# Optimization experiments

Measured on AMD Instinct MI355X. Metric: run time of the kernel, lower is better.

The kernel has to match this reference:

```python
import jax, jax.numpy as jnp
import numpy as np

NEG_SLOPE = 0.2  # PyG GATv2Conv default negative_slope


def setup_inputs() -> dict:
    key = jax.random.key(0)
    ks = jax.random.split(key, 8)
    B, N, C, H, F, E = 16, 5000, 128, 2, 64, 1_280_000
    T = B * N
    s = 0.05
    x = jax.random.normal(ks[0], (B, N, C), jnp.float32)
    edge_index = jax.random.randint(ks[1], (2, E), 0, T, jnp.int32)
    Wl = jax.random.normal(ks[2], (C, H * F), jnp.float32) * s
    bl = jnp.zeros((H * F,), jnp.float32)
    Wr = jax.random.normal(ks[3], (C, H * F), jnp.float32) * s
    br = jnp.zeros((H * F,), jnp.float32)
    att = jax.random.normal(ks[4], (H, F), jnp.float32) * s
    bias = jnp.zeros((H * F,), jnp.float32)
    return {"x": x, "edge_index": edge_index, "Wl": Wl, "bl": bl,
            "Wr": Wr, "br": br, "att": att, "bias": bias}


def reference(x, edge_index, Wl, bl, Wr, br, att, bias):
    # x: (B, N, C) -> flatten to (T, C), T = B*N total nodes
    B, N, C = x.shape
    T = B * N
    H, F = att.shape
    xf = x.reshape(T, C)
    x_l = (xf @ Wl + bl).reshape(T, H, F)  # source transform (lin_l)
    x_r = (xf @ Wr + br).reshape(T, H, F)  # target transform (lin_r)
    # add self loops (add_self_loops=True)
    loops = jnp.arange(T, dtype=edge_index.dtype)
    src = jnp.concatenate([edge_index[0], loops])
    dst = jnp.concatenate([edge_index[1], loops])
    # GATv2 score: att . LeakyReLU(x_j + x_i)
    e = jax.nn.leaky_relu(x_l[src] + x_r[dst], NEG_SLOPE)  # (Et, H, F)
    logits = jnp.einsum('ehf,hf->eh', e, att)              # (Et, H)
    # edge softmax over incoming edges of each dst node
    m = jax.lax.stop_gradient(jax.ops.segment_max(logits, dst, num_segments=T))
    p = jnp.exp(logits - m[dst])
    denom = jax.ops.segment_sum(p, dst, num_segments=T)
    alpha = p / denom[dst]                                  # (Et, H)
    # aggregate: out_i = sum_j alpha_ij * x_l[j]
    out = jax.ops.segment_sum(x_l[src] * alpha[:, :, None], dst, num_segments=T)
    out = out.reshape(T, H * F) + bias  # concat=True -> (T, H*F)
    return out.reshape(B, N, H * F)
```

## Files before the change

kernel.cpp:

```cpp
#include <hip/hip_runtime.h>
#include <hip/hip_bf16.h>

typedef __hip_bfloat16 bf16;
typedef short s16x8 __attribute__((ext_vector_type(8)));
typedef float f32x4 __attribute__((ext_vector_type(4)));
typedef float f32x2 __attribute__((ext_vector_type(2)));

#define NEG_SLOPE 0.2f
#define MAXB 160
#define EPB  4096
#define SCAP 10240
#define TRS  132

__device__ __forceinline__ unsigned int f32_to_bf16_bits(float f) {
    unsigned int u = __float_as_uint(f);
    return (u + 0x7FFFu + ((u >> 16) & 1u)) >> 16;
}
__device__ __forceinline__ float bf16lo_to_f32(unsigned int u) {
    return __uint_as_float(u << 16);
}
__device__ __forceinline__ float bf16hi_to_f32(unsigned int u) {
    return __uint_as_float(u & 0xFFFF0000u);
}
__device__ __forceinline__ float loadf_rt(const void* p, size_t i, int isb) {
    return isb ? __bfloat162float(((const bf16*)p)[i]) : ((const float*)p)[i];
}

#define ROR_ADD(v, n)                                                          \
    v += __int_as_float(__builtin_amdgcn_update_dpp(                           \
        0, __float_as_int(v), 0x120 + (n), 0xF, 0xF, true))

__global__ void prep_w(const unsigned short* __restrict__ xh,
                       const void* __restrict__ Wl, const void* __restrict__ Wr,
                       unsigned short* __restrict__ bpack,
                       int* __restrict__ flag, int* __restrict__ g2)
{
    if (blockIdx.x == 16) {
        int tid = threadIdx.x;
        for (int j = tid; j < 2 * MAXB; j += 256) g2[j] = 0;
        unsigned short h = xh[tid & 255];
        int e = (h >> 7) & 0xFF;
        int c = ((h & 0x7FFF) == 0 || (e >= 117 && e <= 131)) ? 1 : 0;
        __shared__ int sc[4];
        int lane = tid & 63, wid = tid >> 6;
        #pragma unroll
        for (int off = 32; off; off >>= 1) c += __shfl_xor(c, off, 64);
        if (lane == 0) sc[wid] = c;
        __syncthreads();
        if (tid == 0) *flag = ((sc[0] + sc[1] + sc[2] + sc[3]) >= 4 * 192) ? 1 : 0;
        return;
    }

    __shared__ int s_isb;
    {
        int tl = threadIdx.x;
        if (tl < 64) {
            int cnt = 0;
            for (int j = tl; j < 256; j += 64) {
                unsigned short h = xh[j];
                int e = (h >> 7) & 0xFF;
                if ((h & 0x7FFF) == 0 || (e >= 117 && e <= 131)) cnt++;
            }
            #pragma unroll
            for (int off = 32; off; off >>= 1) cnt += __shfl_xor(cnt, off, 64);
            if (tl == 0) s_isb = (cnt >= 192) ? 1 : 0;
        }
        __syncthreads();
    }
    int isb = s_isb;

    int tid = blockIdx.x * 256 + threadIdx.x;
    int lane = tid & 63;
    int kc   = (tid >> 6) & 3;
    int nt   = (tid >> 8) & 7;
    int mat  = tid >> 11;
    const void* W = mat ? Wr : Wl;
    int n  = nt * 16 + (lane & 15);
    int k0 = kc * 32 + (lane >> 4) * 8;
    unsigned short* o = bpack + (size_t)tid * 8;
    #pragma unroll
    for (int j = 0; j < 8; ++j)
        o[j] = (unsigned short)f32_to_bf16_bits(loadf_rt(W, (size_t)(k0 + j) * 128 + n, isb));
}

__global__ void gemm_or_scatter(const void* __restrict__ x,
                                const unsigned short* __restrict__ bpack,
                                const void* __restrict__ bl, const void* __restrict__ br,
                                unsigned int* __restrict__ xlp, unsigned int* __restrict__ xrp,
                                int T, const int* __restrict__ flag,
                                const int* __restrict__ ei, int E, int Et,
                                int nbuck, int Gg, int* __restrict__ delta,
                                unsigned int* __restrict__ packed)
{
    __shared__ unsigned int smem[4][16][TRS];

    if ((int)blockIdx.x >= Gg) {
        int* h   = (int*)&smem[0][0][0];
        int* cur = h + 4 * MAXB;
        int sb  = blockIdx.x - Gg;
        int tid = threadIdx.x, wid = tid >> 6;
        for (int j = tid; j < 4 * MAXB; j += 256) h[j] = 0;
        __syncthreads();
        int start = sb * EPB;
        int end   = min(start + EPB, Et);
        for (int i = start + tid; i < end; i += 256) {
            int dst = (i < E) ? ei[E + i] : (i - E);
            atomicAdd(&h[wid * MAXB + (dst >> 9)], 1);
        }
        __syncthreads();
        for (int b = tid; b < nbuck; b += 256) {
            int c = h[0 * MAXB + b] + h[1 * MAXB + b] + h[2 * MAXB + b] + h[3 * MAXB + b];
            cur[b] = b * SCAP + (c ? atomicAdd(&delta[b], c) : 0);
        }
        __syncthreads();
        for (int i = start + tid; i < end; i += 256) {
            int src, dst;
            if (i < E) { src = ei[i]; dst = ei[E + i]; }
            else       { src = i - E; dst = i - E; }
            int b = dst >> 9;
            int pos = atomicAdd(&cur[b], 1);
            if (pos < (b + 1) * SCAP)
                packed[pos] = ((unsigned int)src << 9) | (unsigned int)(dst & 511);
        }
        return;
    }

    int isb  = *flag;
    int lane = threadIdx.x & 63;
    int wv   = threadIdx.x >> 6;
    int w    = blockIdx.x * 4 + wv;
    int row0 = w * 16;
    if (row0 >= T) return;
    int m = lane & 15, quad = lane >> 4;
    int arow = min(row0 + m, T - 1);

    f32x4 acc[16];
    #pragma unroll
    for (int nt = 0; nt < 16; ++nt) acc[nt] = (f32x4){0.f, 0.f, 0.f, 0.f};

    const s16x8* bp = (const s16x8*)bpack;
    for (int kc = 0; kc < 4; ++kc) {
        s16x8 a;
        if (isb) {
            const unsigned short* xb = (const unsigned short*)x
                                     + (size_t)arow * 128 + kc * 32 + quad * 8;
            a = *(const s16x8*)xb;
        } else {
            const float* xp = (const float*)x + (size_t)arow * 128 + kc * 32 + quad * 8;
            float4 xa = ((const float4*)xp)[0];
            float4 xc = ((const float4*)xp)[1];
            a[0] = (short)f32_to_bf16_bits(xa.x); a[1] = (short)f32_to_bf16_bits(xa.y);
            a[2] = (short)f32_to_bf16_bits(xa.z); a[3] = (short)f32_to_bf16_bits(xa.w);
            a[4] = (short)f32_to_bf16_bits(xc.x); a[5] = (short)f32_to_bf16_bits(xc.y);
            a[6] = (short)f32_to_bf16_bits(xc.z); a[7] = (short)f32_to_bf16_bits(xc.w);
        }
        #pragma unroll
        for (int nt = 0; nt < 16; ++nt) {
            s16x8 b = bp[(size_t)(((nt >> 3) * 32) + (nt & 7) * 4 + kc) * 64 + lane];
            acc[nt] = __builtin_amdgcn_mfma_f32_16x16x32_bf16(a, b, acc[nt], 0, 0, 0);
        }
    }

    #pragma unroll
    for (int nt = 0; nt < 4; ++nt) {
        int fl = nt * 16 + m;
        float bl0 = loadf_rt(bl, fl, isb), bl1 = loadf_rt(bl, 64 + fl, isb);
        float br0 = loadf_rt(br, fl, isb), br1 = loadf_rt(br, 64 + fl, isb);
        #pragma unroll
        for (int r = 0; r < 4; ++r) {
            unsigned int pl = f32_to_bf16_bits(acc[nt][r] + bl0)
                            | (f32_to_bf16_bits(acc[nt + 4][r] + bl1) << 16);
            unsigned int pr = f32_to_bf16_bits(acc[nt + 8][r] + br0)
                            | (f32_to_bf16_bits(acc[nt + 12][r] + br1) << 16);
            smem[wv][quad * 4 + r][fl]      = pl;
            smem[wv][quad * 4 + r][64 + fl] = pr;
        }
    }
    #pragma unroll
    for (int s = 0; s < 4; ++s) {
        int rr = s * 4 + quad;
        int t  = row0 + rr;
        if (t < T) {
            uint4 vl = *(const uint4*)&smem[wv][rr][m * 4];
            uint4 vr = *(const uint4*)&smem[wv][rr][64 + m * 4];
            ((uint4*)(xlp + (size_t)t * 64))[m] = vl;
            ((uint4*)(xrp + (size_t)t * 64))[m] = vr;
        }
    }
}

__global__ void build_csr(unsigned int* __restrict__ packed,
                          const int* __restrict__ delta, int nbuck,
                          int T, int* __restrict__ rowbe)
{
    __shared__ unsigned int st[SCAP];
    __shared__ int h[512];
    __shared__ int off[512];
    __shared__ int ws[4];
    int b    = blockIdx.x;
    int tid  = threadIdx.x, lane = tid & 63, wid = tid >> 6;
    int base = b * SCAP;
    int m    = min(delta[b], SCAP);

    for (int i = tid; i < m; i += 256) st[i] = packed[base + i];
    for (int j = tid; j < 512; j += 256) h[j] = 0;
    __syncthreads();
    for (int i = tid; i < m; i += 256) atomicAdd(&h[st[i] & 511], 1);
    __syncthreads();

    int h0 = h[2 * tid], h1 = h[2 * tid + 1];
    int s  = h0 + h1;
    int xx = s;
    #pragma unroll
    for (int o = 1; o < 64; o <<= 1) {
        int u = __shfl_up(xx, o, 64);
        if (lane >= o) xx += u;
    }
    if (lane == 63) ws[wid] = xx;
    __syncthreads();
    int wo = 0;
    for (int wv = 0; wv < 4; ++wv) if (wv < wid) wo += ws[wv];
    int e0 = wo + xx - s;
    int e1 = e0 + h0;
    off[2 * tid]     = e0;
    off[2 * tid + 1] = e1;
    __syncthreads();
    int e2 = (2 * tid + 2 < 512) ? off[2 * tid + 2] : m;
    int node0 = b * 512 + 2 * tid;
    if (node0 < T) {
        rowbe[2 * node0]     = base + e0;
        rowbe[2 * node0 + 1] = base + e1;
    }
    if (node0 + 1 < T) {
        rowbe[2 * node0 + 2] = base + e1;
        rowbe[2 * node0 + 3] = base + e2;
    }
    __syncthreads();

    for (int i = tid; i < m; i += 256) {
        unsigned int p = st[i];
        int pos = atomicAdd(&off[p & 511], 1);
        packed[base + pos] = p >> 9;
    }
}

__global__ void aggregate(const unsigned int* __restrict__ xlp,
                          const unsigned int* __restrict__ xrp,
                          const int* __restrict__ rowbe, const int* __restrict__ col,
                          const void* __restrict__ att, const void* __restrict__ bias,
                          float* __restrict__ out, int T,
                          const int* __restrict__ flag)
{
    int lane = threadIdx.x & 63;
    int node = blockIdx.x * 8 + (threadIdx.x >> 5);
    if (node >= T) return;
    int isb = *flag;
    int g = (lane >> 4) & 1;
    int q = lane & 15;

    uint4 xr4 = ((const uint4*)(xrp + (size_t)node * 64))[q];
    f32x2 xr2[4], at2[4];
    {
        unsigned int xrw[4] = {xr4.x, xr4.y, xr4.z, xr4.w};
        const float LOG2E = 1.44269504f;
        #pragma unroll
        for (int k = 0; k < 4; ++k) {
            xr2[k] = (f32x2){bf16lo_to_f32(xrw[k]), bf16hi_to_f32(xrw[k])};
            at2[k] = (f32x2){loadf_rt(att, q * 4 + k, isb) * LOG2E,
                             loadf_rt(att, 64 + q * 4 + k, isb) * LOG2E};
        }
    }

    f32x2 s2 = {0.f, 0.f};
    f32x2 a2[4] = {{0.f, 0.f}, {0.f, 0.f}, {0.f, 0.f}, {0.f, 0.f}};

    int2 be = ((const int2*)rowbe)[node];
    int beg = be.x, end = be.y;

    bool v0 = (beg + g) < end;      int sA = v0 ? col[beg + g]     : node;
    bool v1 = (beg + 2 + g) < end;  int sB = v1 ? col[beg + 2 + g] : node;
    bool v2 = (beg + 4 + g) < end;  int sC = v2 ? col[beg + 4 + g] : node;
    uint4 cx = ((const uint4*)(xlp + (size_t)sA * 64))[q];
    uint4 nx = ((const uint4*)(xlp + (size_t)sB * 64))[q];

    for (int i = beg; i < end; i += 2) {
        bool v3 = (i + 6 + g) < end;
        int  sD = v3 ? col[i + 6 + g] : node;
        uint4 px = ((const uint4*)(xlp + (size_t)sC * 64))[q];

        unsigned int xlw[4] = {cx.x, cx.y, cx.z, cx.w};
        f32x2 xl2[4];
        f32x2 t2 = {0.f, 0.f};
        #pragma unroll
        for (int k = 0; k < 4; ++k) {
            xl2[k] = (f32x2){bf16lo_to_f32(xlw[k]), bf16hi_to_f32(xlw[k])};
            f32x2 e  = xl2[k] + xr2[k];
            f32x2 lr = __builtin_elementwise_max(e, e * NEG_SLOPE);
            t2 = __builtin_elementwise_fma(lr, at2[k], t2);
        }
        float t0 = t2.x, t1 = t2.y;
        ROR_ADD(t0, 8); ROR_ADD(t1, 8);
        ROR_ADD(t0, 4); ROR_ADD(t1, 4);
        ROR_ADD(t0, 2); ROR_ADD(t1, 2);
        ROR_ADD(t0, 1); ROR_ADD(t1, 1);
        t0 = fminf(t0, 43.3f);
        t1 = fminf(t1, 43.3f);
        f32x2 p2;
        p2.x = v0 ? exp2f(t0) : 0.f;
        p2.y = v0 ? exp2f(t1) : 0.f;
        s2 += p2;
        #pragma unroll
        for (int k = 0; k < 4; ++k)
            a2[k] = __builtin_elementwise_fma(p2, xl2[k], a2[k]);

        cx = nx; nx = px;
        v0 = v1; v1 = v2; v2 = v3; sC = sD;
    }

    s2.x += __shfl_xor(s2.x, 16, 64);
    s2.y += __shfl_xor(s2.y, 16, 64);
    #pragma unroll
    for (int k = 0; k < 4; ++k) {
        a2[k].x += __shfl_xor(a2[k].x, 16, 64);
        a2[k].y += __shfl_xor(a2[k].y, 16, 64);
    }

    float inv0 = (s2.x > 0.f) ? 1.f / s2.x : 0.f;
    float inv1 = (s2.y > 0.f) ? 1.f / s2.y : 0.f;
    if (g == 0) {
        float4 o;
        o.x = fmaf(a2[0].x, inv0, loadf_rt(bias, q * 4 + 0, isb));
        o.y = fmaf(a2[1].x, inv0, loadf_rt(bias, q * 4 + 1, isb));
        o.z = fmaf(a2[2].x, inv0, loadf_rt(bias, q * 4 + 2, isb));
        o.w = fmaf(a2[3].x, inv0, loadf_rt(bias, q * 4 + 3, isb));
        ((float4*)(out + (size_t)node * 128))[q] = o;
    } else {
        float4 o;
        o.x = fmaf(a2[0].y, inv1, loadf_rt(bias, 64 + q * 4 + 0, isb));
        o.y = fmaf(a2[1].y, inv1, loadf_rt(bias, 64 + q * 4 + 1, isb));
        o.z = fmaf(a2[2].y, inv1, loadf_rt(bias, 64 + q * 4 + 2, isb));
        o.w = fmaf(a2[3].y, inv1, loadf_rt(bias, 64 + q * 4 + 3, isb));
        ((float4*)(out + (size_t)node * 128))[16 + q] = o;
    }
}

extern "C" void kernel_launch(void* const* d_in, const int* in_sizes, int n_in,
                              void* d_out, int out_size, void* d_ws, size_t ws_size,
                              hipStream_t stream)
{
    const void* x    = d_in[0];
    const int*  ei   = (const int*)d_in[1];
    const void* Wl   = d_in[2];
    const void* bl   = d_in[3];
    const void* Wr   = d_in[4];
    const void* br   = d_in[5];
    const void* att  = d_in[6];
    const void* bias = d_in[7];
    float* out = (float*)d_out;

    int T     = in_sizes[0] / 128;
    int E     = in_sizes[1] / 2;
    int Et    = E + T;
    int nbuck = (T + 511) >> 9;
    int nb    = (Et + EPB - 1) / EPB;
    int Gg    = (T + 63) / 64;

    char* w = (char*)d_ws;
    unsigned int* xlp = (unsigned int*)w;  w += (size_t)T * 64 * 4;
    unsigned int* xrp = (unsigned int*)w;  w += (size_t)T * 64 * 4;
    int* rowbe  = (int*)w;  w += (size_t)2 * T * 4;
    unsigned int* packed = (unsigned int*)w;  w += (size_t)nbuck * SCAP * 4;
    int* g2     = (int*)w;  w += 2 * MAXB * 4;
    int* flag   = (int*)w;  w += 256;
    unsigned short* bpack = (unsigned short*)w;  w += 2 * 8 * 4 * 64 * 8 * 2;
    int* delta = g2;

    prep_w<<<17, 256, 0, stream>>>((const unsigned short*)x, Wl, Wr, bpack, flag, g2);
    gemm_or_scatter<<<Gg + nb, 256, 0, stream>>>(x, bpack, bl, br, xlp, xrp, T, flag,
                                                 ei, E, Et, nbuck, Gg, delta, packed);
    build_csr<<<nbuck, 256, 0, stream>>>(packed, delta, nbuck, T, rowbe);

    aggregate<<<(T + 7) / 8, 256, 0, stream>>>(xlp, xrp, rowbe, (const int*)packed,
                                               att, bias, out, T, flag);
}
```

Before: 223.5 us.

## Shrink CSR buckets from 512 to 64 destination nodes per bucket

Reduces the bucketed edge sort granularity from 512 destinations per bucket to 64, giving 1250 buckets with a 1536-entry capacity each instead of 157 buckets of 10240. The scatter histogram becomes a single shared array without per-wave copies, and build_csr now runs one wavefront scan over 64 counters in many small blocks, which increases parallelism and cuts shared-memory use per block. The risks are more global atomics on delta, more contention on the shared histogram, and a bucket capacity that could overflow if in-degree is skewed.

```diff
diff --git a/kernel.cpp b/kernel.cpp
--- a/kernel.cpp
+++ b/kernel.cpp
@@ -7,9 +7,9 @@
 typedef float f32x2 __attribute__((ext_vector_type(2)));
 
 #define NEG_SLOPE 0.2f
-#define MAXB 160
+#define NBMX 1280
 #define EPB  4096
-#define SCAP 10240
+#define SCAP 1536
 #define TRS  132
 
 __device__ __forceinline__ unsigned int f32_to_bf16_bits(float f) {
@@ -33,11 +33,11 @@
 __global__ void prep_w(const unsigned short* __restrict__ xh,
                        const void* __restrict__ Wl, const void* __restrict__ Wr,
                        unsigned short* __restrict__ bpack,
-                       int* __restrict__ flag, int* __restrict__ g2)
+                       int* __restrict__ flag, int* __restrict__ delta)
 {
     if (blockIdx.x == 16) {
         int tid = threadIdx.x;
-        for (int j = tid; j < 2 * MAXB; j += 256) g2[j] = 0;
+        for (int j = tid; j < NBMX; j += 256) delta[j] = 0;
         unsigned short h = xh[tid & 255];
         int e = (h >> 7) & 0xFF;
         int c = ((h & 0x7FFF) == 0 || (e >= 117 && e <= 131)) ? 1 : 0;
@@ -96,20 +96,20 @@
 
     if ((int)blockIdx.x >= Gg) {
         int* h   = (int*)&smem[0][0][0];
-        int* cur = h + 4 * MAXB;
+        int* cur = h + NBMX;
         int sb  = blockIdx.x - Gg;
-        int tid = threadIdx.x, wid = tid >> 6;
-        for (int j = tid; j < 4 * MAXB; j += 256) h[j] = 0;
+        int tid = threadIdx.x;
+        for (int j = tid; j < nbuck; j += 256) h[j] = 0;
         __syncthreads();
         int start = sb * EPB;
         int end   = min(start + EPB, Et);
         for (int i = start + tid; i < end; i += 256) {
             int dst = (i < E) ? ei[E + i] : (i - E);
-            atomicAdd(&h[wid * MAXB + (dst >> 9)], 1);
+            atomicAdd(&h[dst >> 6], 1);
         }
         __syncthreads();
         for (int b = tid; b < nbuck; b += 256) {
-            int c = h[0 * MAXB + b] + h[1 * MAXB + b] + h[2 * MAXB + b] + h[3 * MAXB + b];
+            int c = h[b];
             cur[b] = b * SCAP + (c ? atomicAdd(&delta[b], c) : 0);
         }
         __syncthreads();
@@ -117,10 +117,10 @@
             int src, dst;
             if (i < E) { src = ei[i]; dst = ei[E + i]; }
             else       { src = i - E; dst = i - E; }
-            int b = dst >> 9;
+            int b = dst >> 6;
             int pos = atomicAdd(&cur[b], 1);
             if (pos < (b + 1) * SCAP)
-                packed[pos] = ((unsigned int)src << 9) | (unsigned int)(dst & 511);
+                packed[pos] = ((unsigned int)src << 6) | (unsigned int)(dst & 63);
         }
         return;
     }
@@ -194,53 +194,41 @@
                           int T, int* __restrict__ rowbe)
 {
     __shared__ unsigned int st[SCAP];
-    __shared__ int h[512];
-    __shared__ int off[512];
-    __shared__ int ws[4];
+    __shared__ int h[64];
+    __shared__ int off[64];
     int b    = blockIdx.x;
-    int tid  = threadIdx.x, lane = tid & 63, wid = tid >> 6;
+    int tid  = threadIdx.x;
     int base = b * SCAP;
     int m    = min(delta[b], SCAP);
 
     for (int i = tid; i < m; i += 256) st[i] = packed[base + i];
-    for (int j = tid; j < 512; j += 256) h[j] = 0;
+    if (tid < 64) h[tid] = 0;
     __syncthreads();
-    for (int i = tid; i < m; i += 256) atomicAdd(&h[st[i] & 511], 1);
+    for (int i = tid; i < m; i += 256) atomicAdd(&h[st[i] & 63], 1);
     __syncthreads();
 
-    int h0 = h[2 * tid], h1 = h[2 * tid + 1];
-    int s  = h0 + h1;
-    int xx = s;
-    #pragma unroll
-    for (int o = 1; o < 64; o <<= 1) {
-        int u = __shfl_up(xx, o, 64);
-        if (lane >= o) xx += u;
-    }
-    if (lane == 63) ws[wid] = xx;
-    __syncthreads();
-    int wo = 0;
-    for (int wv = 0; wv < 4; ++wv) if (wv < wid) wo += ws[wv];
-    int e0 = wo + xx - s;
-    int e1 = e0 + h0;
-    off[2 * tid]     = e0;
-    off[2 * tid + 1] = e1;
-    __syncthreads();
-    int e2 = (2 * tid + 2 < 512) ? off[2 * tid + 2] : m;
-    int node0 = b * 512 + 2 * tid;
-    if (node0 < T) {
-        rowbe[2 * node0]     = base + e0;
-        rowbe[2 * node0 + 1] = base + e1;
-    }
-    if (node0 + 1 < T) {
-        rowbe[2 * node0 + 2] = base + e1;
-        rowbe[2 * node0 + 3] = base + e2;
+    if (tid < 64) {
+        int hv  = h[tid];
+        int inc = hv;
+        #pragma unroll
+        for (int o = 1; o < 64; o <<= 1) {
+            int u = __shfl_up(inc, o, 64);
+            if (tid >= o) inc += u;
+        }
+        int excl = inc - hv;
+        off[tid] = excl;
+        int node0 = b * 64 + tid;
+        if (node0 < T) {
+            rowbe[2 * node0]     = base + excl;
+            rowbe[2 * node0 + 1] = base + excl + hv;
+        }
     }
     __syncthreads();
 
     for (int i = tid; i < m; i += 256) {
         unsigned int p = st[i];
-        int pos = atomicAdd(&off[p & 511], 1);
-        packed[base + pos] = p >> 9;
+        int pos = atomicAdd(&off[p & 63], 1);
+        packed[base + pos] = p >> 6;
     }
 }
 
@@ -361,7 +349,7 @@
     int T     = in_sizes[0] / 128;
     int E     = in_sizes[1] / 2;
     int Et    = E + T;
-    int nbuck = (T + 511) >> 9;
+    int nbuck = (T + 63) >> 6;
     int nb    = (Et + EPB - 1) / EPB;
     int Gg    = (T + 63) / 64;
 
@@ -370,12 +358,11 @@
     unsigned int* xrp = (unsigned int*)w;  w += (size_t)T * 64 * 4;
     int* rowbe  = (int*)w;  w += (size_t)2 * T * 4;
     unsigned int* packed = (unsigned int*)w;  w += (size_t)nbuck * SCAP * 4;
-    int* g2     = (int*)w;  w += 2 * MAXB * 4;
+    int* delta  = (int*)w;  w += NBMX * 4;
     int* flag   = (int*)w;  w += 256;
     unsigned short* bpack = (unsigned short*)w;  w += 2 * 8 * 4 * 64 * 8 * 2;
-    int* delta = g2;
-
-    prep_w<<<17, 256, 0, stream>>>((const unsigned short*)x, Wl, Wr, bpack, flag, g2);
+
+    prep_w<<<17, 256, 0, stream>>>((const unsigned short*)x, Wl, Wr, bpack, flag, delta);
     gemm_or_scatter<<<Gg + nb, 256, 0, stream>>>(x, bpack, bl, br, xlp, xrp, T, flag,
                                                  ei, E, Et, nbuck, Gg, delta, packed);
     build_csr<<<nbuck, 256, 0, stream>>>(packed, delta, nbuck, T, rowbe);
```

Result: no change. 223.3 us (-0.1%).
